# Performance work log

Measured on AMD Instinct MI355X. Metric: run time of the kernel, lower is better.

## Reference

```python
import jax, jax.numpy as jnp
import numpy as np

K = 3  # kernel size (hardcoded in module defaults; padding=1, stride=1, dilation=1)


def conv2d(x, w, b, pad=1):
    # x: [B,C,H,W], w: [O,C,kh,kw]
    out = jax.lax.conv_general_dilated(
        x, w, window_strides=(1, 1), padding=[(pad, pad), (pad, pad)],
        dimension_numbers=("NCHW", "OIHW", "NCHW"))
    return out + b[None, :, None, None]


def _bilinear_sample(img, py, px):
    # img: [C,H,W]; py, px: [K*K,Ho,Wo] float sample coords.
    # Zero-padded bilinear sampling (matches torchvision deform_conv2d):
    # each of the 4 corner taps contributes 0 if it lies outside the image.
    H, W = img.shape[1], img.shape[2]
    y0 = jnp.floor(py)
    x0 = jnp.floor(px)
    y1, x1 = y0 + 1.0, x0 + 1.0
    wy1 = py - y0
    wy0 = 1.0 - wy1
    wx1 = px - x0
    wx0 = 1.0 - wx1

    def corner(y, x):
        yi = jnp.clip(y.astype(jnp.int32), 0, H - 1)
        xi = jnp.clip(x.astype(jnp.int32), 0, W - 1)
        valid = ((y >= 0) & (y <= H - 1) & (x >= 0) & (x <= W - 1))
        return img[:, yi, xi] * valid.astype(img.dtype)[None]  # [C,K*K,Ho,Wo]

    return (corner(y0, x0) * (wy0 * wx0)[None]
            + corner(y0, x1) * (wy0 * wx1)[None]
            + corner(y1, x0) * (wy1 * wx0)[None]
            + corner(y1, x1) * (wy1 * wx1)[None])


def setup_inputs() -> dict:
    key = jax.random.key(0)
    ks = jax.random.split(key, 4)
    B, C, O, H, W = 8, 128, 256, 96, 96
    x = jax.random.normal(ks[0], (B, C, H, W), dtype=jnp.float32)
    # scale offset/mask conv weights so learned offsets stay a few pixels
    offset_w = jax.random.normal(ks[1], (2 * K * K, C, K, K), dtype=jnp.float32) * 0.01
    offset_b = jnp.zeros((2 * K * K,), dtype=jnp.float32)
    mask_w = jax.random.normal(ks[2], (K * K, C, K, K), dtype=jnp.float32) * 0.05
    mask_b = jnp.zeros((K * K,), dtype=jnp.float32)
    weight = jax.random.normal(ks[3], (O, C, K, K), dtype=jnp.float32) * 0.05
    bias = jnp.zeros((O,), dtype=jnp.float32)
    return {"x": x, "offset_w": offset_w, "offset_b": offset_b,
            "mask_w": mask_w, "mask_b": mask_b, "weight": weight, "bias": bias}


def reference(x, offset_w, offset_b, mask_w, mask_b, weight, bias):
    B, C, H, W = x.shape
    O = weight.shape[0]
    pad = 1
    offset = conv2d(x, offset_w, offset_b, pad)              # [B,2*K*K,H,W]
    mask = jax.nn.sigmoid(conv2d(x, mask_w, mask_b, pad))    # [B,K*K,H,W]
    Ho, Wo = offset.shape[2], offset.shape[3]

    # base sampling grid: output pixel - pad + kernel tap position
    kh, kw = jnp.meshgrid(jnp.arange(K), jnp.arange(K), indexing="ij")
    kh = kh.reshape(-1).astype(x.dtype)  # [K*K]
    kw = kw.reshape(-1).astype(x.dtype)
    base_y = (jnp.arange(Ho, dtype=x.dtype)[None, :, None] - pad
              + kh[:, None, None])                           # [K*K,Ho,1]
    base_x = (jnp.arange(Wo, dtype=x.dtype)[None, None, :] - pad
              + kw[:, None, None])                           # [K*K,1,Wo]

    # torchvision layout: channel 2k = y-offset, 2k+1 = x-offset for tap k
    off = offset.reshape(B, K * K, 2, Ho, Wo)
    py = base_y[None] + off[:, :, 0]                         # [B,K*K,Ho,Wo]
    px = base_x[None] + off[:, :, 1]

    samples = jax.vmap(_bilinear_sample)(x, py, px)          # [B,C,K*K,Ho,Wo]
    w_flat = weight.reshape(O, C, K * K)
    out = jnp.einsum("bckhw,bkhw,ock->bohw", samples, mask, w_flat)
    return out + bias[None, :, None, None]
```

## Files before the change

### kernel.cpp

```cpp
#include <hip/hip_runtime.h>

#define CIN 128
#define COUT 256
#define IH 96
#define IW 96
#define NB 8
#define HW (IH*IW)
#define NPIX (NB*HW)
#define AST 136
#define BLK_PER_IMG (HW/64)

typedef __attribute__((ext_vector_type(8))) short short8;
typedef __attribute__((ext_vector_type(4))) float floatx4;

static __device__ __forceinline__ short f2bf(float f) {
  unsigned int u = __builtin_bit_cast(unsigned int, f);
  u = u + 0x7fffu + ((u >> 16) & 1u);
  return (short)(u >> 16);
}
static __device__ __forceinline__ float bf2f(short s) {
  unsigned int u = ((unsigned int)(unsigned short)s) << 16;
  return __builtin_bit_cast(float, u);
}

struct Corner {
  float w00, w01, w10, w11;
  const short *r00, *r01, *r10, *r11;
};

static __device__ __forceinline__ Corner corner_setup(float py, float px, float mk,
                                                      const short* xtb, int choff) {
  Corner c;
  float y0f = floorf(py), x0f = floorf(px);
  float wy1 = py - y0f, wx1 = px - x0f;
  float wy0 = 1.f - wy1, wx0 = 1.f - wx1;
  bool vy0 = (y0f >= 0.f) && (y0f <= (float)(IH - 1));
  bool vy1 = (y0f + 1.f >= 0.f) && (y0f + 1.f <= (float)(IH - 1));
  bool vx0 = (x0f >= 0.f) && (x0f <= (float)(IW - 1));
  bool vx1 = (x0f + 1.f >= 0.f) && (x0f + 1.f <= (float)(IW - 1));
  int iy0 = min(max((int)y0f, 0), IH - 1);
  int iy1 = min(max((int)y0f + 1, 0), IH - 1);
  int ix0 = min(max((int)x0f, 0), IW - 1);
  int ix1 = min(max((int)x0f + 1, 0), IW - 1);
  c.w00 = wy0 * wx0 * mk * ((vy0 && vx0) ? 1.f : 0.f);
  c.w01 = wy0 * wx1 * mk * ((vy0 && vx1) ? 1.f : 0.f);
  c.w10 = wy1 * wx0 * mk * ((vy1 && vx0) ? 1.f : 0.f);
  c.w11 = wy1 * wx1 * mk * ((vy1 && vx1) ? 1.f : 0.f);
  c.r00 = xtb + (size_t)(iy0 * IW + ix0) * 128 + choff;
  c.r01 = xtb + (size_t)(iy0 * IW + ix1) * 128 + choff;
  c.r10 = xtb + (size_t)(iy1 * IW + ix0) * 128 + choff;
  c.r11 = xtb + (size_t)(iy1 * IW + ix1) * 128 + choff;
  return c;
}

static __device__ __forceinline__ short8 interp8(short8 s00, short8 s01,
                                                 short8 s10, short8 s11,
                                                 const Corner& c) {
  short8 o;
  #pragma unroll
  for (int j = 0; j < 8; ++j) {
    float v = c.w00 * bf2f(s00[j]) + c.w01 * bf2f(s01[j])
            + c.w10 * bf2f(s10[j]) + c.w11 * bf2f(s11[j]);
    o[j] = f2bf(v);
  }
  return o;
}

__global__ void prep_weights(const float* __restrict__ weight,
                             const float* __restrict__ offset_w,
                             const float* __restrict__ mask_w,
                             short* __restrict__ Bt2f,
                             short* __restrict__ Bt1f) {
  int idx = blockIdx.x * 256 + threadIdx.x;
  const int n2 = 9 * 4 * 16 * 512;
  if (idx < n2) {
    int e = idx & 7, lane = (idx >> 3) & 63;
    int g = idx >> 9;
    int nl = g & 15, kq = (g >> 4) & 3, tap = g >> 6;
    int o = nl * 16 + (lane & 15);
    int c = kq * 32 + (lane >> 4) * 8 + e;
    Bt2f[idx] = f2bf(weight[(o * CIN + c) * 9 + tap]);
  } else {
    int j = idx - n2;
    if (j < 9 * 4 * 2 * 512) {
      int e = j & 7, lane = (j >> 3) & 63;
      int g = j >> 9;
      int nl = g & 1, kq = (g >> 1) & 3, tap = g >> 3;
      int n = nl * 16 + (lane & 15);
      int c = kq * 32 + (lane >> 4) * 8 + e;
      float v = 0.f;
      if (n < 27)
        v = (n < 18) ? offset_w[(n * CIN + c) * 9 + tap]
                     : mask_w[((n - 18) * CIN + c) * 9 + tap];
      Bt1f[j] = f2bf(v);
    }
  }
}

__global__ __launch_bounds__(256, 8)
void transpose_x(const float* __restrict__ x, short* __restrict__ xt) {
  __shared__ short tile[64 * 130];
  const int tid = threadIdx.x;
  const int lane = tid & 63;
  const int wv = tid >> 6;
  const int p0 = blockIdx.x * 64;
  const int b = p0 / HW;
  const int hw0 = p0 % HW;
  const float* xb = x + (size_t)b * CIN * HW + hw0;

  #pragma unroll
  for (int i = 0; i < 32; ++i) {
    int c = wv + i * 4;
    tile[lane * 130 + c] = f2bf(xb[(size_t)c * HW + lane]);
  }
  __syncthreads();

  unsigned int* dst = (unsigned int*)(xt + ((size_t)b * HW + hw0) * 128);
  #pragma unroll
  for (int i = 0; i < 16; ++i) {
    int idx = i * 256 + tid;
    int px = idx >> 6, cw = idx & 63;
    unsigned int lo = (unsigned short)tile[px * 130 + 2 * cw];
    unsigned int hi = (unsigned short)tile[px * 130 + 2 * cw + 1];
    dst[idx] = lo | (hi << 16);
  }
}

__global__ __launch_bounds__(256, 4)
void offmask_kernel(const short* __restrict__ xt,
                    const short* __restrict__ Bt1f,
                    const float* __restrict__ offset_b,
                    const float* __restrict__ mask_b,
                    float* __restrict__ pmt) {
  const int tid  = threadIdx.x;
  const int lane = tid & 63;
  const int wv   = tid >> 6;
  const int q    = lane >> 4;
  const int m    = lane & 15;
  const int blk  = blockIdx.x;
  const int l    = (blk & 7) * BLK_PER_IMG + (blk >> 3);
  const int p0   = l * 64;
  const int b    = p0 / HW;
  const int p    = p0 + wv * 16 + m;
  const int hw   = p % HW;
  const int h    = hw / IW, w_ = hw % IW;
  const short* xtb = xt + (size_t)b * HW * 128;

  floatx4 acc0 = (floatx4){0.f, 0.f, 0.f, 0.f};
  floatx4 acc1 = (floatx4){0.f, 0.f, 0.f, 0.f};

  for (int tap = 0; tap < 9; ++tap) {
    const int kh = tap / 3, kw = tap % 3;
    const int iy = h + kh - 1, ix = w_ + kw - 1;
    const bool vald = (iy >= 0 && iy < IH && ix >= 0 && ix < IW);
    const size_t pbase = vald ? (size_t)(iy * IW + ix) * 128 : 0;

    short8 a[4], bb0[4], bb1[4];
    #pragma unroll
    for (int kq = 0; kq < 4; ++kq)
      a[kq] = *(const short8*)(xtb + pbase + kq * 32 + q * 8);
    #pragma unroll
    for (int kq = 0; kq < 4; ++kq) {
      bb0[kq] = *(const short8*)(Bt1f + (size_t)((tap * 4 + kq) * 2 + 0) * 512 + lane * 8);
      bb1[kq] = *(const short8*)(Bt1f + (size_t)((tap * 4 + kq) * 2 + 1) * 512 + lane * 8);
    }
    #pragma unroll
    for (int kq = 0; kq < 4; ++kq) {
      short8 av = a[kq];
      if (!vald) av = (short8){0, 0, 0, 0, 0, 0, 0, 0};
      acc0 = __builtin_amdgcn_mfma_f32_16x16x32_bf16(av, bb0[kq], acc0, 0, 0, 0);
      acc1 = __builtin_amdgcn_mfma_f32_16x16x32_bf16(av, bb1[kq], acc1, 0, 0, 0);
    }
  }

  #pragma unroll
  for (int nl = 0; nl < 2; ++nl) {
    floatx4 ac = nl ? acc1 : acc0;
    int ch = nl * 16 + m;
    if (ch < 18) {
      int tap = ch >> 1, plane = ch & 1;
      float cb = offset_b[ch];
      #pragma unroll
      for (int r = 0; r < 4; ++r) {
        int pp = p0 + wv * 16 + q * 4 + r;
        int hwp = pp % HW;
        float base = plane ? (float)(hwp % IW + tap % 3 - 1)
                           : (float)(hwp / IW + tap / 3 - 1);
        pmt[(size_t)(plane * 9 + tap) * NPIX + pp] = ac[r] + cb + base;
      }
    } else if (ch < 27) {
      int tap = ch - 18;
      float cb = mask_b[tap];
      #pragma unroll
      for (int r = 0; r < 4; ++r) {
        int pp = p0 + wv * 16 + q * 4 + r;
        float v = ac[r] + cb;
        pmt[(size_t)(18 + tap) * NPIX + pp] = 1.f / (1.f + expf(-v));
      }
    }
  }
}

__global__ __launch_bounds__(256, 2)
void deform_main(const short* __restrict__ xt,
                 const short* __restrict__ Bt2f,
                 const float* __restrict__ pmt,
                 const float* __restrict__ bias,
                 float* __restrict__ out) {
  __shared__ short Ald[2][64 * AST];

  const int tid  = threadIdx.x;
  const int lane = tid & 63;
  const int wv   = tid >> 6;
  const int q    = lane >> 4;
  const int m    = lane & 15;
  const int blk  = blockIdx.x;
  const int l    = (blk & 7) * BLK_PER_IMG + (blk >> 3);
  const int p0   = l * 64;
  const int b    = p0 / HW;
  const short* xtb = xt + (size_t)b * HW * 128;

  const int r8    = lane >> 3;
  const int ck    = lane & 7;
  const int ckoff = ck * 8;
  const int row0  = wv * 16 + r8;
  const int row1  = row0 + 8;
  const int p_s0  = p0 + row0;
  const int p_s1  = p0 + row1;
  const int wk0   = (row0 >> 1) & 7;
  const int wk1   = (row1 >> 1) & 7;
  const int wb0   = row0 * AST;
  const int wb1   = row1 * AST;
  const int rsw   = (m >> 1) & 7;

  floatx4 acc[4][4];
  #pragma unroll
  for (int i = 0; i < 4; ++i)
    #pragma unroll
    for (int j = 0; j < 4; ++j) acc[i][j] = (floatx4){0.f, 0.f, 0.f, 0.f};

  {
    float py0 = pmt[p_s0], px0 = pmt[(size_t)9 * NPIX + p_s0], mk0 = pmt[(size_t)18 * NPIX + p_s0];
    float py1 = pmt[p_s1], px1 = pmt[(size_t)9 * NPIX + p_s1], mk1 = pmt[(size_t)18 * NPIX + p_s1];
    Corner c0 = corner_setup(py0, px0, mk0, xtb, ckoff);
    Corner c1 = corner_setup(py1, px1, mk1, xtb, ckoff);
    short8 a0 = *(const short8*)(c0.r00),      a1 = *(const short8*)(c0.r01);
    short8 a2 = *(const short8*)(c0.r10),      a3 = *(const short8*)(c0.r11);
    short8 a4 = *(const short8*)(c0.r00 + 64), a5 = *(const short8*)(c0.r01 + 64);
    short8 a6 = *(const short8*)(c0.r10 + 64), a7 = *(const short8*)(c0.r11 + 64);
    short8 b0 = *(const short8*)(c1.r00),      b1 = *(const short8*)(c1.r01);
    short8 b2 = *(const short8*)(c1.r10),      b3 = *(const short8*)(c1.r11);
    short8 b4 = *(const short8*)(c1.r00 + 64), b5 = *(const short8*)(c1.r01 + 64);
    short8 b6 = *(const short8*)(c1.r10 + 64), b7 = *(const short8*)(c1.r11 + 64);
    *(short8*)(&Ald[0][wb0 + (ck ^ wk0) * 8])       = interp8(a0, a1, a2, a3, c0);
    *(short8*)(&Ald[0][wb0 + (8 + (ck ^ wk0)) * 8]) = interp8(a4, a5, a6, a7, c0);
    *(short8*)(&Ald[0][wb1 + (ck ^ wk1) * 8])       = interp8(b0, b1, b2, b3, c1);
    *(short8*)(&Ald[0][wb1 + (8 + (ck ^ wk1)) * 8]) = interp8(b4, b5, b6, b7, c1);
  }
  float pyN0 = pmt[(size_t)1 * NPIX + p_s0];
  float pxN0 = pmt[(size_t)10 * NPIX + p_s0];
  float mkN0 = pmt[(size_t)19 * NPIX + p_s0];
  float pyN1 = pmt[(size_t)1 * NPIX + p_s1];
  float pxN1 = pmt[(size_t)10 * NPIX + p_s1];
  float mkN1 = pmt[(size_t)19 * NPIX + p_s1];
  __syncthreads();

  for (int tap = 0; tap < 9; ++tap) {
    const short* bufr = Ald[tap & 1];
    short* const wbuf = Ald[(tap & 1) ^ 1];
    const bool nxt = (tap < 8);

    Corner c0, c1;
    if (nxt) {
      c0 = corner_setup(pyN0, pxN0, mkN0, xtb, ckoff);
      c1 = corner_setup(pyN1, pxN1, mkN1, xtb, ckoff);
    }
    if (tap < 7) {
      pyN0 = pmt[(size_t)(tap + 2) * NPIX + p_s0];
      pxN0 = pmt[(size_t)(tap + 11) * NPIX + p_s0];
      mkN0 = pmt[(size_t)(tap + 20) * NPIX + p_s0];
      pyN1 = pmt[(size_t)(tap + 2) * NPIX + p_s1];
      pxN1 = pmt[(size_t)(tap + 11) * NPIX + p_s1];
      mkN1 = pmt[(size_t)(tap + 20) * NPIX + p_s1];
    }

    short8 bfA[4], bfB[4];
    #pragma unroll
    for (int nl = 0; nl < 4; ++nl) {
      bfA[nl] = *(const short8*)(Bt2f + (size_t)((tap * 4 + 0) * 16 + wv * 4 + nl) * 512 + lane * 8);
      bfB[nl] = *(const short8*)(Bt2f + (size_t)((tap * 4 + 1) * 16 + wv * 4 + nl) * 512 + lane * 8);
    }
    short8 g0, g1, g2, g3, g4, g5, g6, g7;
    if (nxt) {
      g0 = *(const short8*)(c0.r00);      g1 = *(const short8*)(c0.r01);
      g2 = *(const short8*)(c0.r10);      g3 = *(const short8*)(c0.r11);
      g4 = *(const short8*)(c0.r00 + 64); g5 = *(const short8*)(c0.r01 + 64);
      g6 = *(const short8*)(c0.r10 + 64); g7 = *(const short8*)(c0.r11 + 64);
    }
    {
      short8 af[4];
      #pragma unroll
      for (int mt = 0; mt < 4; ++mt)
        af[mt] = *(const short8*)(bufr + (mt * 16 + m) * AST + ((0 * 4 + q) ^ rsw) * 8);
      #pragma unroll
      for (int mt = 0; mt < 4; ++mt)
        #pragma unroll
        for (int nl = 0; nl < 4; ++nl)
          acc[mt][nl] = __builtin_amdgcn_mfma_f32_16x16x32_bf16(af[mt], bfA[nl], acc[mt][nl], 0, 0, 0);
    }
    {
      short8 af[4];
      #pragma unroll
      for (int mt = 0; mt < 4; ++mt)
        af[mt] = *(const short8*)(bufr + (mt * 16 + m) * AST + ((1 * 4 + q) ^ rsw) * 8);
      #pragma unroll
      for (int mt = 0; mt < 4; ++mt)
        #pragma unroll
        for (int nl = 0; nl < 4; ++nl)
          acc[mt][nl] = __builtin_amdgcn_mfma_f32_16x16x32_bf16(af[mt], bfB[nl], acc[mt][nl], 0, 0, 0);
    }
    short8 bfC[4], bfD[4];
    #pragma unroll
    for (int nl = 0; nl < 4; ++nl) {
      bfC[nl] = *(const short8*)(Bt2f + (size_t)((tap * 4 + 2) * 16 + wv * 4 + nl) * 512 + lane * 8);
      bfD[nl] = *(const short8*)(Bt2f + (size_t)((tap * 4 + 3) * 16 + wv * 4 + nl) * 512 + lane * 8);
    }
    if (nxt) {
      *(short8*)(&wbuf[wb0 + (ck ^ wk0) * 8])       = interp8(g0, g1, g2, g3, c0);
      *(short8*)(&wbuf[wb0 + (8 + (ck ^ wk0)) * 8]) = interp8(g4, g5, g6, g7, c0);
      g0 = *(const short8*)(c1.r00);      g1 = *(const short8*)(c1.r01);
      g2 = *(const short8*)(c1.r10);      g3 = *(const short8*)(c1.r11);
      g4 = *(const short8*)(c1.r00 + 64); g5 = *(const short8*)(c1.r01 + 64);
      g6 = *(const short8*)(c1.r10 + 64); g7 = *(const short8*)(c1.r11 + 64);
    }
    {
      short8 af[4];
      #pragma unroll
      for (int mt = 0; mt < 4; ++mt)
        af[mt] = *(const short8*)(bufr + (mt * 16 + m) * AST + ((2 * 4 + q) ^ rsw) * 8);
      #pragma unroll
      for (int mt = 0; mt < 4; ++mt)
        #pragma unroll
        for (int nl = 0; nl < 4; ++nl)
          acc[mt][nl] = __builtin_amdgcn_mfma_f32_16x16x32_bf16(af[mt], bfC[nl], acc[mt][nl], 0, 0, 0);
    }
    {
      short8 af[4];
      #pragma unroll
      for (int mt = 0; mt < 4; ++mt)
        af[mt] = *(const short8*)(bufr + (mt * 16 + m) * AST + ((3 * 4 + q) ^ rsw) * 8);
      #pragma unroll
      for (int mt = 0; mt < 4; ++mt)
        #pragma unroll
        for (int nl = 0; nl < 4; ++nl)
          acc[mt][nl] = __builtin_amdgcn_mfma_f32_16x16x32_bf16(af[mt], bfD[nl], acc[mt][nl], 0, 0, 0);
    }
    if (nxt) {
      *(short8*)(&wbuf[wb1 + (ck ^ wk1) * 8])       = interp8(g0, g1, g2, g3, c1);
      *(short8*)(&wbuf[wb1 + (8 + (ck ^ wk1)) * 8]) = interp8(g4, g5, g6, g7, c1);
      __syncthreads();
    }
  }

  const int hw0 = p0 % HW;
  #pragma unroll
  for (int nl = 0; nl < 4; ++nl) {
    const int o = wv * 64 + nl * 16 + m;
    const float bs = bias[o];
    float* op = out + (size_t)(b * COUT + o) * HW + hw0;
    #pragma unroll
    for (int mt = 0; mt < 4; ++mt) {
      floatx4 v = acc[mt][nl];
      v[0] += bs; v[1] += bs; v[2] += bs; v[3] += bs;
      *(floatx4*)(op + mt * 16 + q * 4) = v;
    }
  }
}

extern "C" void kernel_launch(void* const* d_in, const int* in_sizes, int n_in,
                              void* d_out, int out_size, void* d_ws, size_t ws_size,
                              hipStream_t stream) {
  const float* x        = (const float*)d_in[0];
  const float* offset_w = (const float*)d_in[1];
  const float* offset_b = (const float*)d_in[2];
  const float* mask_w   = (const float*)d_in[3];
  const float* mask_b   = (const float*)d_in[4];
  const float* weight   = (const float*)d_in[5];
  const float* bias     = (const float*)d_in[6];
  float* out = (float*)d_out;

  char* ws = (char*)d_ws;
  const size_t XT_BYTES  = (size_t)NPIX * 128 * 2;
  const size_t PMT_BYTES = (size_t)27 * NPIX * 4;
  const size_t BT2_BYTES = (size_t)9 * 4 * 16 * 512 * 2;
  short* xtp  = (short*)ws;
  float* pmt  = (float*)(ws + XT_BYTES);
  short* Bt2f = (short*)(ws + XT_BYTES + PMT_BYTES);
  short* Bt1f = (short*)(ws + XT_BYTES + PMT_BYTES + BT2_BYTES);

  prep_weights<<<dim3(1296), dim3(256), 0, stream>>>(weight, offset_w, mask_w, Bt2f, Bt1f);
  transpose_x<<<dim3(NPIX / 64), dim3(256), 0, stream>>>(x, xtp);
  offmask_kernel<<<dim3(NPIX / 64), dim3(256), 0, stream>>>(xtp, Bt1f, offset_b, mask_b, pmt);
  deform_main<<<dim3(NPIX / 64), dim3(256), 0, stream>>>(xtp, Bt2f, pmt, bias, out);
}
```

Baseline: 225.6 us.

## Fuse offset/mask convolution into deform kernel via shared-memory staging

Removes the separate offset/mask kernel and computes the 27-channel offset and mask conv at the start of each deform_main block, storing results in a padded shared-memory buffer instead of a global pmt array. This drops one kernel launch and the global write and re-read of the offset/mask planes. It also raises launch bounds to 3 blocks per SM. Those two changes together may raise register pressure in the fused kernel and add a prologue before the main gather/MFMA loop.

Measured after the change: 221.4 us. About the same (-1.9%).

```diff
diff --git a/kernel.cpp b/kernel.cpp
--- a/kernel.cpp
+++ b/kernel.cpp
@@ -126,88 +126,16 @@
   }
 }
 
-__global__ __launch_bounds__(256, 4)
-void offmask_kernel(const short* __restrict__ xt,
-                    const short* __restrict__ Bt1f,
-                    const float* __restrict__ offset_b,
-                    const float* __restrict__ mask_b,
-                    float* __restrict__ pmt) {
-  const int tid  = threadIdx.x;
-  const int lane = tid & 63;
-  const int wv   = tid >> 6;
-  const int q    = lane >> 4;
-  const int m    = lane & 15;
-  const int blk  = blockIdx.x;
-  const int l    = (blk & 7) * BLK_PER_IMG + (blk >> 3);
-  const int p0   = l * 64;
-  const int b    = p0 / HW;
-  const int p    = p0 + wv * 16 + m;
-  const int hw   = p % HW;
-  const int h    = hw / IW, w_ = hw % IW;
-  const short* xtb = xt + (size_t)b * HW * 128;
-
-  floatx4 acc0 = (floatx4){0.f, 0.f, 0.f, 0.f};
-  floatx4 acc1 = (floatx4){0.f, 0.f, 0.f, 0.f};
-
-  for (int tap = 0; tap < 9; ++tap) {
-    const int kh = tap / 3, kw = tap % 3;
-    const int iy = h + kh - 1, ix = w_ + kw - 1;
-    const bool vald = (iy >= 0 && iy < IH && ix >= 0 && ix < IW);
-    const size_t pbase = vald ? (size_t)(iy * IW + ix) * 128 : 0;
-
-    short8 a[4], bb0[4], bb1[4];
-    #pragma unroll
-    for (int kq = 0; kq < 4; ++kq)
-      a[kq] = *(const short8*)(xtb + pbase + kq * 32 + q * 8);
-    #pragma unroll
-    for (int kq = 0; kq < 4; ++kq) {
-      bb0[kq] = *(const short8*)(Bt1f + (size_t)((tap * 4 + kq) * 2 + 0) * 512 + lane * 8);
-      bb1[kq] = *(const short8*)(Bt1f + (size_t)((tap * 4 + kq) * 2 + 1) * 512 + lane * 8);
-    }
-    #pragma unroll
-    for (int kq = 0; kq < 4; ++kq) {
-      short8 av = a[kq];
-      if (!vald) av = (short8){0, 0, 0, 0, 0, 0, 0, 0};
-      acc0 = __builtin_amdgcn_mfma_f32_16x16x32_bf16(av, bb0[kq], acc0, 0, 0, 0);
-      acc1 = __builtin_amdgcn_mfma_f32_16x16x32_bf16(av, bb1[kq], acc1, 0, 0, 0);
-    }
-  }
-
-  #pragma unroll
-  for (int nl = 0; nl < 2; ++nl) {
-    floatx4 ac = nl ? acc1 : acc0;
-    int ch = nl * 16 + m;
-    if (ch < 18) {
-      int tap = ch >> 1, plane = ch & 1;
-      float cb = offset_b[ch];
-      #pragma unroll
-      for (int r = 0; r < 4; ++r) {
-        int pp = p0 + wv * 16 + q * 4 + r;
-        int hwp = pp % HW;
-        float base = plane ? (float)(hwp % IW + tap % 3 - 1)
-                           : (float)(hwp / IW + tap / 3 - 1);
-        pmt[(size_t)(plane * 9 + tap) * NPIX + pp] = ac[r] + cb + base;
-      }
-    } else if (ch < 27) {
-      int tap = ch - 18;
-      float cb = mask_b[tap];
-      #pragma unroll
-      for (int r = 0; r < 4; ++r) {
-        int pp = p0 + wv * 16 + q * 4 + r;
-        float v = ac[r] + cb;
-        pmt[(size_t)(18 + tap) * NPIX + pp] = 1.f / (1.f + expf(-v));
-      }
-    }
-  }
-}
-
-__global__ __launch_bounds__(256, 2)
+__global__ __launch_bounds__(256, 3)
 void deform_main(const short* __restrict__ xt,
                  const short* __restrict__ Bt2f,
-                 const float* __restrict__ pmt,
+                 const short* __restrict__ Bt1f,
+                 const float* __restrict__ offset_b,
+                 const float* __restrict__ mask_b,
                  const float* __restrict__ bias,
                  float* __restrict__ out) {
   __shared__ short Ald[2][64 * AST];
+  __shared__ float pmb[27 * 65];
 
   const int tid  = threadIdx.x;
   const int lane = tid & 63;
@@ -220,13 +148,72 @@
   const int b    = p0 / HW;
   const short* xtb = xt + (size_t)b * HW * 128;
 
+  {
+    const int p  = p0 + wv * 16 + m;
+    const int hw = p % HW;
+    const int h  = hw / IW, w_ = hw % IW;
+
+    floatx4 acc0 = (floatx4){0.f, 0.f, 0.f, 0.f};
+    floatx4 acc1 = (floatx4){0.f, 0.f, 0.f, 0.f};
+
+    for (int tap = 0; tap < 9; ++tap) {
+      const int kh = tap / 3, kw = tap % 3;
+      const int iy = h + kh - 1, ix = w_ + kw - 1;
+      const bool vald = (iy >= 0 && iy < IH && ix >= 0 && ix < IW);
+      const size_t pbase = vald ? (size_t)(iy * IW + ix) * 128 : 0;
+
+      short8 a[4], bb0[4], bb1[4];
+      #pragma unroll
+      for (int kq = 0; kq < 4; ++kq)
+        a[kq] = *(const short8*)(xtb + pbase + kq * 32 + q * 8);
+      #pragma unroll
+      for (int kq = 0; kq < 4; ++kq) {
+        bb0[kq] = *(const short8*)(Bt1f + (size_t)((tap * 4 + kq) * 2 + 0) * 512 + lane * 8);
+        bb1[kq] = *(const short8*)(Bt1f + (size_t)((tap * 4 + kq) * 2 + 1) * 512 + lane * 8);
+      }
+      #pragma unroll
+      for (int kq = 0; kq < 4; ++kq) {
+        short8 av = a[kq];
+        if (!vald) av = (short8){0, 0, 0, 0, 0, 0, 0, 0};
+        acc0 = __builtin_amdgcn_mfma_f32_16x16x32_bf16(av, bb0[kq], acc0, 0, 0, 0);
+        acc1 = __builtin_amdgcn_mfma_f32_16x16x32_bf16(av, bb1[kq], acc1, 0, 0, 0);
+      }
+    }
+
+    #pragma unroll
+    for (int nl = 0; nl < 2; ++nl) {
+      floatx4 ac = nl ? acc1 : acc0;
+      int ch = nl * 16 + m;
+      if (ch < 18) {
+        int tap = ch >> 1, plane = ch & 1;
+        float cb = offset_b[ch];
+        #pragma unroll
+        for (int r = 0; r < 4; ++r) {
+          int col = wv * 16 + q * 4 + r;
+          int hwp = (p0 + col) % HW;
+          float base = plane ? (float)(hwp % IW + tap % 3 - 1)
+                             : (float)(hwp / IW + tap / 3 - 1);
+          pmb[(plane * 9 + tap) * 65 + col] = ac[r] + cb + base;
+        }
+      } else if (ch < 27) {
+        int tap = ch - 18;
+        float cb = mask_b[tap];
+        #pragma unroll
+        for (int r = 0; r < 4; ++r) {
+          int col = wv * 16 + q * 4 + r;
+          float v = ac[r] + cb;
+          pmb[(18 + tap) * 65 + col] = 1.f / (1.f + expf(-v));
+        }
+      }
+    }
+  }
+  __syncthreads();
+
   const int r8    = lane >> 3;
   const int ck    = lane & 7;
   const int ckoff = ck * 8;
   const int row0  = wv * 16 + r8;
   const int row1  = row0 + 8;
-  const int p_s0  = p0 + row0;
-  const int p_s1  = p0 + row1;
   const int wk0   = (row0 >> 1) & 7;
   const int wk1   = (row1 >> 1) & 7;
   const int wb0   = row0 * AST;
@@ -240,8 +227,8 @@
     for (int j = 0; j < 4; ++j) acc[i][j] = (floatx4){0.f, 0.f, 0.f, 0.f};
 
   {
-    float py0 = pmt[p_s0], px0 = pmt[(size_t)9 * NPIX + p_s0], mk0 = pmt[(size_t)18 * NPIX + p_s0];
-    float py1 = pmt[p_s1], px1 = pmt[(size_t)9 * NPIX + p_s1], mk1 = pmt[(size_t)18 * NPIX + p_s1];
+    float py0 = pmb[row0], px0 = pmb[9 * 65 + row0], mk0 = pmb[18 * 65 + row0];
+    float py1 = pmb[row1], px1 = pmb[9 * 65 + row1], mk1 = pmb[18 * 65 + row1];
     Corner c0 = corner_setup(py0, px0, mk0, xtb, ckoff);
     Corner c1 = corner_setup(py1, px1, mk1, xtb, ckoff);
     short8 a0 = *(const short8*)(c0.r00),      a1 = *(const short8*)(c0.r01);
@@ -257,12 +244,12 @@
     *(short8*)(&Ald[0][wb1 + (ck ^ wk1) * 8])       = interp8(b0, b1, b2, b3, c1);
     *(short8*)(&Ald[0][wb1 + (8 + (ck ^ wk1)) * 8]) = interp8(b4, b5, b6, b7, c1);
   }
-  float pyN0 = pmt[(size_t)1 * NPIX + p_s0];
-  float pxN0 = pmt[(size_t)10 * NPIX + p_s0];
-  float mkN0 = pmt[(size_t)19 * NPIX + p_s0];
-  float pyN1 = pmt[(size_t)1 * NPIX + p_s1];
-  float pxN1 = pmt[(size_t)10 * NPIX + p_s1];
-  float mkN1 = pmt[(size_t)19 * NPIX + p_s1];
+  float pyN0 = pmb[1 * 65 + row0];
+  float pxN0 = pmb[10 * 65 + row0];
+  float mkN0 = pmb[19 * 65 + row0];
+  float pyN1 = pmb[1 * 65 + row1];
+  float pxN1 = pmb[10 * 65 + row1];
+  float mkN1 = pmb[19 * 65 + row1];
   __syncthreads();
 
   for (int tap = 0; tap < 9; ++tap) {
@@ -276,12 +263,12 @@
       c1 = corner_setup(pyN1, pxN1, mkN1, xtb, ckoff);
     }
     if (tap < 7) {
-      pyN0 = pmt[(size_t)(tap + 2) * NPIX + p_s0];
-      pxN0 = pmt[(size_t)(tap + 11) * NPIX + p_s0];
-      mkN0 = pmt[(size_t)(tap + 20) * NPIX + p_s0];
-      pyN1 = pmt[(size_t)(tap + 2) * NPIX + p_s1];
-      pxN1 = pmt[(size_t)(tap + 11) * NPIX + p_s1];
-      mkN1 = pmt[(size_t)(tap + 20) * NPIX + p_s1];
+      pyN0 = pmb[(tap + 2) * 65 + row0];
+      pxN0 = pmb[(tap + 11) * 65 + row0];
+      mkN0 = pmb[(tap + 20) * 65 + row0];
+      pyN1 = pmb[(tap + 2) * 65 + row1];
+      pxN1 = pmb[(tap + 11) * 65 + row1];
+      mkN1 = pmb[(tap + 20) * 65 + row1];
     }
 
     short8 bfA[4], bfB[4];
@@ -391,15 +378,12 @@
 
   char* ws = (char*)d_ws;
   const size_t XT_BYTES  = (size_t)NPIX * 128 * 2;
-  const size_t PMT_BYTES = (size_t)27 * NPIX * 4;
   const size_t BT2_BYTES = (size_t)9 * 4 * 16 * 512 * 2;
   short* xtp  = (short*)ws;
-  float* pmt  = (float*)(ws + XT_BYTES);
-  short* Bt2f = (short*)(ws + XT_BYTES + PMT_BYTES);
-  short* Bt1f = (short*)(ws + XT_BYTES + PMT_BYTES + BT2_BYTES);
+  short* Bt2f = (short*)(ws + XT_BYTES);
+  short* Bt1f = (short*)(ws + XT_BYTES + BT2_BYTES);
 
   prep_weights<<<dim3(1296), dim3(256), 0, stream>>>(weight, offset_w, mask_w, Bt2f, Bt1f);
   transpose_x<<<dim3(NPIX / 64), dim3(256), 0, stream>>>(x, xtp);
-  offmask_kernel<<<dim3(NPIX / 64), dim3(256), 0, stream>>>(xtp, Bt1f, offset_b, mask_b, pmt);
-  deform_main<<<dim3(NPIX / 64), dim3(256), 0, stream>>>(xtp, Bt2f, pmt, bias, out);
-}
+  deform_main<<<dim3(NPIX / 64), dim3(256), 0, stream>>>(xtp, Bt2f, Bt1f, offset_b, mask_b, bias, out);
+}
```
